# Kernel tuning notes

Measured on AMD Instinct MI355X. Metric: run time of the kernel, lower is better.

The kernel has to match this reference:

```python
import jax, jax.numpy as jnp
import numpy as np

N = 100000
DEG = 16            # edges per source node (1 self-loop + 15 random)
E = N * DEG
IN_F = 128
OUT_F = 64
ALPHA = 0.2         # leaky relu negative slope


def _build_edges(key):
    # edges sorted by src (as adj.nonzero() would be), every node has >=1 out-edge
    src = jnp.repeat(jnp.arange(N, dtype=jnp.int32), DEG)
    dst = jax.random.randint(key, (E,), 0, N, dtype=jnp.int32)
    # force a self-loop as the first edge of every block
    self_pos = jnp.arange(E, dtype=jnp.int32) % DEG == 0
    dst = jnp.where(self_pos, src, dst)
    return jnp.stack([src, dst])  # [2, E]


def setup_inputs() -> dict:
    key = jax.random.key(0)
    k1, k2, k3, k4, k5, k6 = jax.random.split(key, 6)
    return {
        "input": jax.random.normal(k1, (N, IN_F), dtype=jnp.float32),
        "edge": _build_edges(k2),
        "W_high": jax.random.normal(k3, (IN_F, OUT_F), dtype=jnp.float32) * 0.1,
        "W_low": jax.random.normal(k4, (IN_F, OUT_F), dtype=jnp.float32) * 0.1,
        "a_high": jax.random.normal(k5, (1, 2 * OUT_F), dtype=jnp.float32) * 0.1,
        "a_low": jax.random.normal(k6, (1, 2 * OUT_F), dtype=jnp.float32) * 0.1,
    }


def _relu6(x):
    return jnp.clip(x, 0.0, 6.0)


def reference(input, edge, W_high, W_low, a_high, a_low):
    n = input.shape[0]
    src, dst = edge[0], edge[1]

    h_high = input @ W_high          # [N, F]
    h_low = input @ W_low            # [N, F]

    # a.mm(cat(h[src], h[dst]).T) == (h @ a_src)[src] + (h @ a_dst)[dst]
    f = W_high.shape[1]
    s_high = (h_high @ a_high[0, :f])[src] + (h_high @ a_high[0, f:])[dst]  # [E]
    s_low = (h_low @ a_low[0, :f])[src] + (h_low @ a_low[0, f:])[dst]

    edge_e_high = jnp.exp(-jax.nn.leaky_relu(s_high, ALPHA))  # [E], > 0
    edge_e_low = jnp.exp(-jax.nn.leaky_relu(s_low, ALPHA))

    seg = lambda v: jax.ops.segment_sum(v, src, num_segments=n, indices_are_sorted=True)

    # rowsum uses RAW exp values (before relu6/dropout), matching the source
    e_high_rowsum = seg(edge_e_high)[:, None]  # [N, 1]
    e_low_rowsum = seg(edge_e_low)[:, None]

    # relu6 clamp (dropout p=0 -> identity, eval mode)
    eh = _relu6(edge_e_high)
    el = _relu6(edge_e_low)

    # m @ (h[src] +/- h[dst]) == segment_sum over src of per-edge features
    h_agg_high = seg(h_high[src] + h_high[dst])   # [N, F]
    h_agg_low = seg(h_low[src] - h_low[dst])      # [N, F]

    # spmm: out[i] = sum_{(i,j)} e_ij * h_agg[j]
    h_prime_high = seg(eh[:, None] * h_agg_high[dst]) / e_high_rowsum
    h_prime_low = seg(el[:, None] * h_agg_low[dst]) / e_low_rowsum

    h_prime = 0.5 * (h_prime_high + h_prime_low)
    return _relu6(h_prime)  # concat=True
```

## Files before the change

kernel.cpp:

```cpp
#include <hip/hip_runtime.h>

#define N_NODES 100000
#define DEG 16
#define IN_F 128
#define OUT_F 64
#define E_EDGES (N_NODES * DEG)
#define TILES 1563
#define GEMM_GRID 768

typedef __bf16 bf16x8 __attribute__((ext_vector_type(8)));
typedef unsigned short u16x8 __attribute__((ext_vector_type(8)));
typedef float f32x4 __attribute__((ext_vector_type(4)));
typedef unsigned int u32x4 __attribute__((ext_vector_type(4)));

union BF8 { u16x8 u; bf16x8 b; };

__device__ inline float lo_bf(unsigned int u) {
    union { unsigned int i; float f; } v; v.i = u << 16; return v.f;
}
__device__ inline float hi_bf(unsigned int u) {
    union { unsigned int i; float f; } v; v.i = u & 0xFFFF0000u; return v.f;
}
__device__ inline unsigned short f2bf(float f) {
    union { float f; unsigned int i; } v; v.f = f;
    return (unsigned short)((v.i + 0x7FFFu + ((v.i >> 16) & 1u)) >> 16);
}
__device__ inline unsigned int packbf(float a, float b) {
    return (unsigned int)f2bf(a) | ((unsigned int)f2bf(b) << 16);
}

__global__ __launch_bounds__(256) void k_gemm(
    const float* __restrict__ in, const float* __restrict__ Wh,
    const float* __restrict__ Wl, unsigned int* __restrict__ H)
{
    __shared__ __align__(16) unsigned short ldsW[2][64][136];
    __shared__ __align__(16) unsigned short ldsA[64][136];

    {
        int n  = threadIdx.x & 63;
        int kg = threadIdx.x >> 6;
        #pragma unroll
        for (int m = 0; m < 2; m++) {
            const float* W = m ? Wl : Wh;
            #pragma unroll
            for (int i = 0; i < 32; i += 2) {
                int k = kg * 32 + i;
                float a = W[k * 64 + n];
                float b = W[(k + 1) * 64 + n];
                *(unsigned int*)&ldsW[m][n][k] = packbf(a, b);
            }
        }
    }

    int wv = threadIdx.x >> 6;
    int lane = threadIdx.x & 63;
    int quad = lane >> 4, c = lane & 15;

    f32x4 av[8];
    int tile = blockIdx.x;
    if (tile >= TILES) return;

    {
        int row0B = tile * 64;
        const f32x4* src = (const f32x4*)(in + (size_t)row0B * IN_F);
        #pragma unroll
        for (int i = 0; i < 8; i++) {
            int cch = threadIdx.x + 256 * i;
            int row = cch >> 5;
            int kc = (cch & 31) * 4;
            int grow = row0B + row;
            av[i] = (grow < N_NODES) ? src[cch]
                    : *(const f32x4*)(in + (size_t)(N_NODES - 1) * IN_F + kc);
        }
    }

    for (; tile < TILES; tile += GEMM_GRID) {
        int row0B = tile * 64;

        __syncthreads();
        #pragma unroll
        for (int i = 0; i < 8; i++) {
            int cch = threadIdx.x + 256 * i;
            int row = cch >> 5;
            int kc = (cch & 31) * 4;
            *(unsigned int*)&ldsA[row][kc]     = packbf(av[i][0], av[i][1]);
            *(unsigned int*)&ldsA[row][kc + 2] = packbf(av[i][2], av[i][3]);
        }
        __syncthreads();

        int ntile = tile + GEMM_GRID;
        if (ntile < TILES) {
            int nrow0 = ntile * 64;
            const f32x4* src = (const f32x4*)(in + (size_t)nrow0 * IN_F);
            #pragma unroll
            for (int i = 0; i < 8; i++) {
                int cch = threadIdx.x + 256 * i;
                int row = cch >> 5;
                int kc = (cch & 31) * 4;
                int grow = nrow0 + row;
                av[i] = (grow < N_NODES) ? src[cch]
                        : *(const f32x4*)(in + (size_t)(N_NODES - 1) * IN_F + kc);
            }
        }

        bf16x8 afrag[4];
        #pragma unroll
        for (int kb = 0; kb < 4; kb++) {
            BF8 a;
            a.u = *(const u16x8*)&ldsA[wv * 16 + c][kb * 32 + quad * 8];
            afrag[kb] = a.b;
        }

        f32x4 acc[2][4];
        #pragma unroll
        for (int m = 0; m < 2; m++)
            #pragma unroll
            for (int t = 0; t < 4; t++) acc[m][t] = (f32x4){0, 0, 0, 0};

        #pragma unroll
        for (int kb = 0; kb < 4; kb++) {
            #pragma unroll
            for (int t = 0; t < 4; t++) {
                int n = t * 16 + c;
                BF8 bh, bl;
                bh.u = *(const u16x8*)&ldsW[0][n][kb * 32 + quad * 8];
                bl.u = *(const u16x8*)&ldsW[1][n][kb * 32 + quad * 8];
                acc[0][t] = __builtin_amdgcn_mfma_f32_16x16x32_bf16(afrag[kb], bh.b, acc[0][t], 0, 0, 0);
                acc[1][t] = __builtin_amdgcn_mfma_f32_16x16x32_bf16(afrag[kb], bl.b, acc[1][t], 0, 0, 0);
            }
        }

        int row0 = row0B + wv * 16;
        #pragma unroll
        for (int r = 0; r < 4; r++) {
            int row = row0 + quad * 4 + r;
            if (row >= N_NODES) continue;
            size_t base = (size_t)row * OUT_F + c;
            #pragma unroll
            for (int t = 0; t < 4; t++)
                H[base + t * 16] = packbf(acc[0][t][r], acc[1][t][r]);
        }
    }
}

__global__ __launch_bounds__(256) void k_agg(
    const unsigned int* __restrict__ H, const int* __restrict__ dst,
    const float* __restrict__ ah, const float* __restrict__ al,
    unsigned int* __restrict__ HAGG, f32x4* __restrict__ s)
{
    int lane = threadIdx.x & 63;
    int node = __builtin_amdgcn_readfirstlane(blockIdx.x * 4 + (threadIdx.x >> 6));
    const int* dp = dst + node * DEG;

    unsigned int hu = H[(size_t)node * 64 + lane];
    float hh = lo_bf(hu);
    float hl = hi_bf(hu);
    float sh = 16.0f * hh;
    float sl = 16.0f * hl;

    #pragma unroll
    for (int half = 0; half < 2; half++) {
        unsigned int u[8];
        #pragma unroll
        for (int t = 0; t < 8; t++) {
            int j = dp[half * 8 + t];
            u[t] = H[(size_t)j * 64 + lane];
        }
        #pragma unroll
        for (int t = 0; t < 8; t++) { sh += lo_bf(u[t]); sl -= hi_bf(u[t]); }
    }
    HAGG[(size_t)node * 64 + lane] = packbf(sh, sl);

    float ph = hh * ah[lane];
    float qh = hh * ah[64 + lane];
    float pl = hl * al[lane];
    float ql = hl * al[64 + lane];
    #pragma unroll
    for (int o = 32; o > 0; o >>= 1) {
        ph += __shfl_xor(ph, o);
        qh += __shfl_xor(qh, o);
        pl += __shfl_xor(pl, o);
        ql += __shfl_xor(ql, o);
    }
    if (lane == 0) s[node] = (f32x4){ph, qh, pl, ql};
}

__global__ __launch_bounds__(256) void k_out(
    const unsigned int* __restrict__ HAGG, const int* __restrict__ dst,
    const f32x4* __restrict__ s, float* __restrict__ out)
{
    int lane = threadIdx.x & 63;
    int node = __builtin_amdgcn_readfirstlane(blockIdx.x * 4 + (threadIdx.x >> 6));
    const int* dp = dst + node * DEG;

    int jl = dp[lane & 15];
    f32x4 si = s[node];
    f32x4 sj = s[jl];
    float xh = si.x + sj.y;
    float xl = si.z + sj.w;
    float lh = xh > 0.0f ? xh : 0.2f * xh;
    float ll = xl > 0.0f ? xl : 0.2f * xl;
    float wh = __expf(-lh);
    float wl = __expf(-ll);
    float rh = wh, rl = wl;
    #pragma unroll
    for (int o = 8; o > 0; o >>= 1) { rh += __shfl_xor(rh, o); rl += __shfl_xor(rl, o); }
    float eh = fminf(wh, 6.0f);
    float el = fminf(wl, 6.0f);

    float acc_h = 0.0f, acc_l = 0.0f;
    #pragma unroll
    for (int half = 0; half < 2; half++) {
        unsigned int u[8];
        float weh[8], wel[8];
        #pragma unroll
        for (int t = 0; t < 8; t++) {
            int j = dp[half * 8 + t];
            u[t] = HAGG[(size_t)j * 64 + lane];
        }
        #pragma unroll
        for (int t = 0; t < 8; t++) {
            weh[t] = __shfl(eh, half * 8 + t);
            wel[t] = __shfl(el, half * 8 + t);
        }
        #pragma unroll
        for (int t = 0; t < 8; t++) {
            acc_h += weh[t] * lo_bf(u[t]);
            acc_l += wel[t] * hi_bf(u[t]);
        }
    }
    float r = 0.5f * (acc_h / rh + acc_l / rl);
    r = fminf(fmaxf(r, 0.0f), 6.0f);
    out[(size_t)node * 64 + lane] = r;
}

extern "C" void kernel_launch(void* const* d_in, const int* in_sizes, int n_in,
                              void* d_out, int out_size, void* d_ws, size_t ws_size,
                              hipStream_t stream) {
    const float* input = (const float*)d_in[0];
    const int*   edge  = (const int*)d_in[1];
    const float* Wh    = (const float*)d_in[2];
    const float* Wl    = (const float*)d_in[3];
    const float* ah    = (const float*)d_in[4];
    const float* al    = (const float*)d_in[5];
    float* out = (float*)d_out;

    unsigned int* H    = (unsigned int*)d_ws;
    unsigned int* HAGG = H + (size_t)N_NODES * 64;
    f32x4* s = (f32x4*)(HAGG + (size_t)N_NODES * 64);

    const int* dstp = edge + E_EDGES;

    k_gemm<<<GEMM_GRID, 256, 0, stream>>>(input, Wh, Wl, H);
    k_agg<<<N_NODES / 4, 256, 0, stream>>>(H, dstp, ah, al, HAGG, s);
    k_out<<<N_NODES / 4, 256, 0, stream>>>(HAGG, dstp, s, out);
}
```

Measured before the change: 225.8 us.

## Fuse GEMM, aggregation and output into one cooperative persistent kernel

Replaces the three separate launches with a single cooperative kernel that runs the GEMM, neighbor aggregation and attention-weighted output phases, separated by fenced grid-wide barriers. The GEMM phase now builds A fragments directly from global memory instead of staging them through LDS with software prefetch. The aim is to remove launch overhead and inter-kernel gaps. In exchange it adds grid-sync cost and a persistent grid sized from occupancy (capped at 2048 blocks), and keeps the old three-kernel path as a fallback.

```diff
diff --git a/kernel.cpp b/kernel.cpp
--- a/kernel.cpp
+++ b/kernel.cpp
@@ -1,4 +1,7 @@
 #include <hip/hip_runtime.h>
+#include <hip/hip_cooperative_groups.h>
+
+namespace cg = cooperative_groups;
 
 #define N_NODES 100000
 #define DEG 16
@@ -28,6 +31,186 @@
 __device__ inline unsigned int packbf(float a, float b) {
     return (unsigned int)f2bf(a) | ((unsigned int)f2bf(b) << 16);
 }
+
+__device__ inline bf16x8 mk_afrag(const float* ap) {
+    f32x4 a0 = *(const f32x4*)ap;
+    f32x4 a1 = *(const f32x4*)(ap + 4);
+    BF8 r;
+    r.u[0] = f2bf(a0[0]); r.u[1] = f2bf(a0[1]);
+    r.u[2] = f2bf(a0[2]); r.u[3] = f2bf(a0[3]);
+    r.u[4] = f2bf(a1[0]); r.u[5] = f2bf(a1[1]);
+    r.u[6] = f2bf(a1[2]); r.u[7] = f2bf(a1[3]);
+    return r.b;
+}
+
+__device__ inline void grid_sync_fenced() {
+    __builtin_amdgcn_fence(__ATOMIC_RELEASE, "agent");
+    cg::this_grid().sync();
+    __builtin_amdgcn_fence(__ATOMIC_ACQUIRE, "agent");
+}
+
+__global__ __launch_bounds__(256, 4) void k_fused(
+    const float* __restrict__ in, const float* __restrict__ Wh,
+    const float* __restrict__ Wl, const int* __restrict__ dst,
+    const float* __restrict__ ah, const float* __restrict__ al,
+    unsigned int* __restrict__ H, unsigned int* __restrict__ HAGG,
+    f32x4* __restrict__ s, float* __restrict__ out)
+{
+    __shared__ __align__(16) unsigned short ldsW[2][64][136];
+    const int stride = gridDim.x;
+
+    {
+        int n  = threadIdx.x & 63;
+        int kg = threadIdx.x >> 6;
+        #pragma unroll
+        for (int m = 0; m < 2; m++) {
+            const float* W = m ? Wl : Wh;
+            #pragma unroll
+            for (int i = 0; i < 32; i += 2) {
+                int k = kg * 32 + i;
+                float a = W[k * 64 + n];
+                float b = W[(k + 1) * 64 + n];
+                *(unsigned int*)&ldsW[m][n][k] = packbf(a, b);
+            }
+        }
+    }
+    __syncthreads();
+
+    int wv = threadIdx.x >> 6;
+    int lane = threadIdx.x & 63;
+    int quad = lane >> 4, c = lane & 15;
+
+    for (int tile = blockIdx.x; tile < TILES; tile += stride) {
+        int row0B = tile * 64;
+        int arow = row0B + wv * 16 + c;
+        const float* ap = in + (size_t)(arow < N_NODES ? arow : N_NODES - 1) * IN_F;
+
+        bf16x8 afrag[4];
+        #pragma unroll
+        for (int kb = 0; kb < 4; kb++)
+            afrag[kb] = mk_afrag(ap + kb * 32 + quad * 8);
+
+        f32x4 acc[2][4];
+        #pragma unroll
+        for (int m = 0; m < 2; m++)
+            #pragma unroll
+            for (int t = 0; t < 4; t++) acc[m][t] = (f32x4){0, 0, 0, 0};
+
+        #pragma unroll
+        for (int kb = 0; kb < 4; kb++) {
+            #pragma unroll
+            for (int t = 0; t < 4; t++) {
+                int n = t * 16 + c;
+                BF8 bh, bl;
+                bh.u = *(const u16x8*)&ldsW[0][n][kb * 32 + quad * 8];
+                bl.u = *(const u16x8*)&ldsW[1][n][kb * 32 + quad * 8];
+                acc[0][t] = __builtin_amdgcn_mfma_f32_16x16x32_bf16(afrag[kb], bh.b, acc[0][t], 0, 0, 0);
+                acc[1][t] = __builtin_amdgcn_mfma_f32_16x16x32_bf16(afrag[kb], bl.b, acc[1][t], 0, 0, 0);
+            }
+        }
+
+        int row0 = row0B + wv * 16;
+        #pragma unroll
+        for (int r = 0; r < 4; r++) {
+            int row = row0 + quad * 4 + r;
+            if (row >= N_NODES) continue;
+            size_t base = (size_t)row * OUT_F + c;
+            #pragma unroll
+            for (int t = 0; t < 4; t++)
+                H[base + t * 16] = packbf(acc[0][t][r], acc[1][t][r]);
+        }
+    }
+
+    float a0 = ah[lane], a1 = ah[64 + lane];
+    float c0 = al[lane], c1 = al[64 + lane];
+
+    grid_sync_fenced();
+
+    for (int grp = blockIdx.x; grp < N_NODES / 4; grp += stride) {
+        int node = __builtin_amdgcn_readfirstlane(grp * 4 + wv);
+        const int* dp = dst + node * DEG;
+
+        unsigned int hu = H[(size_t)node * 64 + lane];
+        float hh = lo_bf(hu);
+        float hl = hi_bf(hu);
+        float sh = 16.0f * hh;
+        float sl = 16.0f * hl;
+
+        #pragma unroll
+        for (int half = 0; half < 2; half++) {
+            unsigned int u[8];
+            #pragma unroll
+            for (int t = 0; t < 8; t++) {
+                int j = dp[half * 8 + t];
+                u[t] = H[(size_t)j * 64 + lane];
+            }
+            #pragma unroll
+            for (int t = 0; t < 8; t++) { sh += lo_bf(u[t]); sl -= hi_bf(u[t]); }
+        }
+        HAGG[(size_t)node * 64 + lane] = packbf(sh, sl);
+
+        float ph = hh * a0;
+        float qh = hh * a1;
+        float pl = hl * c0;
+        float ql = hl * c1;
+        #pragma unroll
+        for (int o = 32; o > 0; o >>= 1) {
+            ph += __shfl_xor(ph, o);
+            qh += __shfl_xor(qh, o);
+            pl += __shfl_xor(pl, o);
+            ql += __shfl_xor(ql, o);
+        }
+        if (lane == 0) s[node] = (f32x4){ph, qh, pl, ql};
+    }
+
+    grid_sync_fenced();
+
+    for (int grp = blockIdx.x; grp < N_NODES / 4; grp += stride) {
+        int node = __builtin_amdgcn_readfirstlane(grp * 4 + wv);
+        const int* dp = dst + node * DEG;
+
+        int jl = dp[lane & 15];
+        f32x4 si = s[node];
+        f32x4 sj = s[jl];
+        float xh = si.x + sj.y;
+        float xl = si.z + sj.w;
+        float lh = xh > 0.0f ? xh : 0.2f * xh;
+        float ll = xl > 0.0f ? xl : 0.2f * xl;
+        float wh = __expf(-lh);
+        float wl = __expf(-ll);
+        float rh = wh, rl = wl;
+        #pragma unroll
+        for (int o = 8; o > 0; o >>= 1) { rh += __shfl_xor(rh, o); rl += __shfl_xor(rl, o); }
+        float eh = fminf(wh, 6.0f);
+        float el = fminf(wl, 6.0f);
+
+        float acc_h = 0.0f, acc_l = 0.0f;
+        #pragma unroll
+        for (int half = 0; half < 2; half++) {
+            unsigned int u[8];
+            float weh[8], wel[8];
+            #pragma unroll
+            for (int t = 0; t < 8; t++) {
+                int j = dp[half * 8 + t];
+                u[t] = HAGG[(size_t)j * 64 + lane];
+            }
+            #pragma unroll
+            for (int t = 0; t < 8; t++) {
+                weh[t] = __shfl(eh, half * 8 + t);
+                wel[t] = __shfl(el, half * 8 + t);
+            }
+            #pragma unroll
+            for (int t = 0; t < 8; t++) {
+                acc_h += weh[t] * lo_bf(u[t]);
+                acc_l += wel[t] * hi_bf(u[t]);
+            }
+        }
+        float r = 0.5f * (acc_h / rh + acc_l / rl);
+        r = fminf(fmaxf(r, 0.0f), 6.0f);
+        out[(size_t)node * 64 + lane] = r;
+    }
+}
+
 
 __global__ __launch_bounds__(256) void k_gemm(
     const float* __restrict__ in, const float* __restrict__ Wh,
@@ -251,7 +434,30 @@
 
     const int* dstp = edge + E_EDGES;
 
-    k_gemm<<<GEMM_GRID, 256, 0, stream>>>(input, Wh, Wl, H);
-    k_agg<<<N_NODES / 4, 256, 0, stream>>>(H, dstp, ah, al, HAGG, s);
-    k_out<<<N_NODES / 4, 256, 0, stream>>>(HAGG, dstp, s, out);
-}
+    static int coopGrid = -1;
+    if (coopGrid < 0) {
+        int mb = 0;
+        if (hipOccupancyMaxActiveBlocksPerMultiprocessor(
+                &mb, reinterpret_cast<const void*>(&k_fused), 256, 0) != hipSuccess)
+            mb = 0;
+        coopGrid = mb * 256;
+        if (coopGrid > 2048) coopGrid = 2048;
+    }
+
+    bool launched = false;
+    if (coopGrid >= 256) {
+        void* args[] = { (void*)&input, (void*)&Wh, (void*)&Wl, (void*)&dstp,
+                         (void*)&ah, (void*)&al, (void*)&H, (void*)&HAGG,
+                         (void*)&s, (void*)&out };
+        if (hipLaunchCooperativeKernel(reinterpret_cast<const void*>(&k_fused),
+                                       dim3(coopGrid), dim3(256),
+                                       args, 0, stream) == hipSuccess)
+            launched = true;
+    }
+
+    if (!launched) {
+        k_gemm<<<GEMM_GRID, 256, 0, stream>>>(input, Wh, Wl, H);
+        k_agg<<<N_NODES / 4, 256, 0, stream>>>(H, dstp, ah, al, HAGG, s);
+        k_out<<<N_NODES / 4, 256, 0, stream>>>(HAGG, dstp, s, out);
+    }
+}
```

After: 523.9 us. 132% more time.
